# Performance work log

Measured on AMD Instinct MI355X. Metric: run time of the kernel, lower is better.

Reference implementation:

```python
import jax, jax.numpy as jnp
import numpy as np

B, D, R, E, L = 8192, 2048, 64, 4, 3


def setup_inputs() -> dict:
    key = jax.random.key(0)
    ks = jax.random.split(key, 6)
    inputs = jax.random.normal(ks[0], (B, D), dtype=jnp.float32)
    # xavier-normal-ish init for low-rank factors
    U = jax.random.normal(ks[1], (L, E, D, R), dtype=jnp.float32) * (2.0 / (D + R)) ** 0.5
    V = jax.random.normal(ks[2], (L, E, D, R), dtype=jnp.float32) * (2.0 / (D + R)) ** 0.5
    C = jax.random.normal(ks[3], (L, E, R, R), dtype=jnp.float32) * (1.0 / R) ** 0.5
    gate_w = jax.random.normal(ks[4], (E, D), dtype=jnp.float32) * (1.0 / D) ** 0.5
    bias = jnp.zeros((L, D), dtype=jnp.float32)
    return {"inputs": inputs, "U": U, "V": V, "C": C, "gate_w": gate_w, "bias": bias}


def reference(inputs, U, V, C, gate_w, bias):
    x0 = inputs                      # (B, D)
    x_l = inputs
    for i in range(L):
        # gating scores per expert, softmax over experts
        gs = jax.nn.softmax(x_l @ gate_w.T, axis=-1)            # (B, E)
        # low-rank cross: tanh(V^T x) -> tanh(C .) -> U .
        vx = jnp.tanh(jnp.einsum('edr,bd->ber', V[i], x_l))     # (B, E, R)
        cx = jnp.tanh(jnp.einsum('esr,ber->bes', C[i], vx))     # (B, E, R)
        uv = jnp.einsum('eds,bes->bed', U[i], cx)               # (B, E, D)
        dot = (uv + bias[i][None, None, :]) * x0[:, None, :]    # (B, E, D)
        x_l = jnp.einsum('bed,be->bd', dot, gs) + x_l           # MoE combine + residual
    return x_l
```

## Files before the change

### kernel.cpp

```cpp
#include <hip/hip_runtime.h>
#include <cmath>

#define Bb 8192
#define Dd 2048
#define Rr 64
#define Ee 4
#define Ll 3

typedef __bf16 bf16x8 __attribute__((ext_vector_type(8)));
typedef float f32x4 __attribute__((ext_vector_type(4)));
typedef unsigned short u16x8 __attribute__((ext_vector_type(8)));
typedef unsigned short u16x4 __attribute__((ext_vector_type(4)));

__device__ __forceinline__ unsigned short f2bf(float f){
  unsigned u = __builtin_bit_cast(unsigned, f);
  u += 0x7fffu + ((u >> 16) & 1u);
  return (unsigned short)(u >> 16);
}
__device__ __forceinline__ float bf2f(unsigned short h){
  return __builtin_bit_cast(float, ((unsigned)h) << 16);
}

__global__ __launch_bounds__(256) void cast_x_k(const float* __restrict__ x,
                                                unsigned short* __restrict__ xb0){
  const int n4 = Bb * Dd / 4;
  for (int i = blockIdx.x * blockDim.x + threadIdx.x; i < n4; i += gridDim.x * blockDim.x){
    f32x4 v = *((const f32x4*)x + i);
    u16x4 o;
    o[0] = f2bf(v[0]); o[1] = f2bf(v[1]); o[2] = f2bf(v[2]); o[3] = f2bf(v[3]);
    *((u16x4*)xb0 + i) = o;
  }
}

__global__ __launch_bounds__(256) void prep_w_k(const float* __restrict__ U,
                                                const float* __restrict__ V,
                                                const float* __restrict__ C,
                                                const float* __restrict__ gw,
                                                unsigned short* __restrict__ VfT,
                                                unsigned short* __restrict__ UfT,
                                                unsigned short* __restrict__ cb16,
                                                unsigned short* __restrict__ gw16){
  const int NV = Ll * 256 * Dd;
  const int NU = Ll * Dd * 256;
  const int NC = Ll * Ee * Rr * Rr;
  const int NG = Ee * Dd;
  const int total = NV + NU + NC + NG;
  for (int idx = blockIdx.x * blockDim.x + threadIdx.x; idx < total; idx += gridDim.x * blockDim.x){
    if (idx < NV){
      int l = idx / (256 * Dd); int rem = idx - l * 256 * Dd;
      int n = rem / Dd, d = rem - n * Dd;
      int e = n >> 6, r = n & 63;
      VfT[idx] = f2bf(V[(((size_t)l * Ee + e) * Dd + d) * Rr + r]);
    } else if (idx < NV + NU){
      int j = idx - NV;
      int l = j / (Dd * 256); int rem = j - l * Dd * 256;
      int d = rem / 256, k = rem - d * 256;
      int e = k >> 6, s = k & 63;
      UfT[j] = f2bf(U[(((size_t)l * Ee + e) * Dd + d) * Rr + s]);
    } else if (idx < NV + NU + NC){
      int j = idx - NV - NU;
      cb16[j] = f2bf(C[j]);
    } else {
      int j = idx - NV - NU - NC;
      gw16[j] = f2bf(gw[j]);
    }
  }
}

template<bool AF32>
__global__ __launch_bounds__(256) void gate_k(const void* __restrict__ xv,
                                              const unsigned short* __restrict__ gw16,
                                              float* __restrict__ gs){
  const int lane = threadIdx.x & 63;
  const int w = threadIdx.x >> 6;
  const int row = blockIdx.x * 4 + w;
  float s0 = 0.f, s1 = 0.f, s2 = 0.f, s3 = 0.f;
  #pragma unroll
  for (int c = 0; c < 4; c++){
    const int k = c * 512 + lane * 8;
    float xf[8];
    if constexpr (AF32){
      const float* xr = (const float*)xv + (size_t)row * Dd + k;
      f32x4 v0 = *(const f32x4*)xr;
      f32x4 v1 = *(const f32x4*)(xr + 4);
      #pragma unroll
      for (int u = 0; u < 4; u++){ xf[u] = v0[u]; xf[4 + u] = v1[u]; }
    } else {
      u16x8 xvv = *(const u16x8*)((const unsigned short*)xv + (size_t)row * Dd + k);
      #pragma unroll
      for (int u = 0; u < 8; u++) xf[u] = bf2f(xvv[u]);
    }
    u16x8 g0v = *(const u16x8*)(gw16 + 0 * Dd + k);
    u16x8 g1v = *(const u16x8*)(gw16 + 1 * Dd + k);
    u16x8 g2v = *(const u16x8*)(gw16 + 2 * Dd + k);
    u16x8 g3v = *(const u16x8*)(gw16 + 3 * Dd + k);
    #pragma unroll
    for (int u = 0; u < 8; u++){
      s0 += xf[u] * bf2f(g0v[u]);
      s1 += xf[u] * bf2f(g1v[u]);
      s2 += xf[u] * bf2f(g2v[u]);
      s3 += xf[u] * bf2f(g3v[u]);
    }
  }
  #pragma unroll
  for (int m = 1; m < 64; m <<= 1){
    s0 += __shfl_xor(s0, m, 64);
    s1 += __shfl_xor(s1, m, 64);
    s2 += __shfl_xor(s2, m, 64);
    s3 += __shfl_xor(s3, m, 64);
  }
  if (lane == 0){
    float mx = fmaxf(fmaxf(s0, s1), fmaxf(s2, s3));
    float e0 = __expf(s0 - mx), e1 = __expf(s1 - mx), e2 = __expf(s2 - mx), e3 = __expf(s3 - mx);
    float inv = 1.f / (e0 + e1 + e2 + e3);
    f32x4 g; g[0] = e0 * inv; g[1] = e1 * inv; g[2] = e2 * inv; g[3] = e3 * inv;
    *(f32x4*)(gs + (size_t)row * 4) = g;
  }
}

template<bool AF32>
__global__ __launch_bounds__(256) void gemm1_k(const void* __restrict__ Av,
                                               const unsigned short* __restrict__ BT,
                                               unsigned short* __restrict__ vxp){
  const int bm0 = blockIdx.x * 64;
  const int bn0 = blockIdx.y * 128;
  const int z   = blockIdx.z;
  const int kc0 = z * 512;
  const int tid = threadIdx.x;
  const int lane = tid & 63;
  const int wv = tid >> 6;
  const int wm = wv >> 1, wn = wv & 1;

  __shared__ __align__(16) char smraw[27648];
  unsigned short (*As)[72] = (unsigned short (*)[72])smraw;
  unsigned short (*Bs)[72] = (unsigned short (*)[72])(smraw + 9216);
  float (*epi)[132] = (float (*)[132])smraw;

  f32x4 acc[2][4] = {};
  const int arow = tid >> 2;
  const int aseg = tid & 3;

  const float* Af = (const float*)Av;
  const unsigned short* Ab = (const unsigned short*)Av;

  f32x4 a4[4]; u16x8 ar[2]; u16x8 br[4];
  if constexpr (AF32){
    #pragma unroll
    for (int j = 0; j < 4; j++)
      a4[j] = *(const f32x4*)(Af + (size_t)(bm0 + arow) * Dd + kc0 + aseg * 16 + j * 4);
  } else {
    ar[0] = *(const u16x8*)(Ab + (size_t)(bm0 + arow) * Dd + kc0 + aseg * 16);
    ar[1] = *(const u16x8*)(Ab + (size_t)(bm0 + arow) * Dd + kc0 + aseg * 16 + 8);
  }
  br[0] = *(const u16x8*)(BT + (size_t)(bn0 + arow) * Dd + kc0 + aseg * 16);
  br[1] = *(const u16x8*)(BT + (size_t)(bn0 + arow) * Dd + kc0 + aseg * 16 + 8);
  br[2] = *(const u16x8*)(BT + (size_t)(bn0 + arow + 64) * Dd + kc0 + aseg * 16);
  br[3] = *(const u16x8*)(BT + (size_t)(bn0 + arow + 64) * Dd + kc0 + aseg * 16 + 8);

  for (int k0 = kc0; k0 < kc0 + 512; k0 += 64){
    __syncthreads();
    if constexpr (AF32){
      u16x8 av0, av1;
      #pragma unroll
      for (int j = 0; j < 4; j++){
        av0[j] = f2bf(a4[0][j]); av0[4 + j] = f2bf(a4[1][j]);
        av1[j] = f2bf(a4[2][j]); av1[4 + j] = f2bf(a4[3][j]);
      }
      *(u16x8*)(&As[arow][aseg * 16])     = av0;
      *(u16x8*)(&As[arow][aseg * 16 + 8]) = av1;
    } else {
      *(u16x8*)(&As[arow][aseg * 16])     = ar[0];
      *(u16x8*)(&As[arow][aseg * 16 + 8]) = ar[1];
    }
    *(u16x8*)(&Bs[arow][aseg * 16])          = br[0];
    *(u16x8*)(&Bs[arow][aseg * 16 + 8])      = br[1];
    *(u16x8*)(&Bs[arow + 64][aseg * 16])     = br[2];
    *(u16x8*)(&Bs[arow + 64][aseg * 16 + 8]) = br[3];
    __syncthreads();

    int kn = k0 + 64;
    if (kn < kc0 + 512){
      if constexpr (AF32){
        #pragma unroll
        for (int j = 0; j < 4; j++)
          a4[j] = *(const f32x4*)(Af + (size_t)(bm0 + arow) * Dd + kn + aseg * 16 + j * 4);
      } else {
        ar[0] = *(const u16x8*)(Ab + (size_t)(bm0 + arow) * Dd + kn + aseg * 16);
        ar[1] = *(const u16x8*)(Ab + (size_t)(bm0 + arow) * Dd + kn + aseg * 16 + 8);
      }
      br[0] = *(const u16x8*)(BT + (size_t)(bn0 + arow) * Dd + kn + aseg * 16);
      br[1] = *(const u16x8*)(BT + (size_t)(bn0 + arow) * Dd + kn + aseg * 16 + 8);
      br[2] = *(const u16x8*)(BT + (size_t)(bn0 + arow + 64) * Dd + kn + aseg * 16);
      br[3] = *(const u16x8*)(BT + (size_t)(bn0 + arow + 64) * Dd + kn + aseg * 16 + 8);
    }

    #pragma unroll
    for (int ks = 0; ks < 2; ks++){
      bf16x8 af[2];
      #pragma unroll
      for (int mi = 0; mi < 2; mi++)
        af[mi] = *reinterpret_cast<const bf16x8*>(&As[wm * 32 + mi * 16 + (lane & 15)][ks * 32 + (lane >> 4) * 8]);
      #pragma unroll
      for (int nj = 0; nj < 4; nj++){
        bf16x8 bfr = *reinterpret_cast<const bf16x8*>(&Bs[wn * 64 + nj * 16 + (lane & 15)][ks * 32 + (lane >> 4) * 8]);
        #pragma unroll
        for (int mi = 0; mi < 2; mi++)
          acc[mi][nj] = __builtin_amdgcn_mfma_f32_16x16x32_bf16(af[mi], bfr, acc[mi][nj], 0, 0, 0);
      }
    }
  }

  unsigned short* outz = vxp + (size_t)z * Bb * 256;
  #pragma unroll
  for (int h = 0; h < 2; h++){
    __syncthreads();
    if (wm == h){
      #pragma unroll
      for (int mi = 0; mi < 2; mi++)
        #pragma unroll
        for (int nj = 0; nj < 4; nj++)
          #pragma unroll
          for (int q = 0; q < 4; q++)
            epi[mi * 16 + (lane >> 4) * 4 + q][wn * 64 + nj * 16 + (lane & 15)] = acc[mi][nj][q];
    }
    __syncthreads();
    #pragma unroll
    for (int c = 0; c < 4; c++){
      int idx = c * 256 + tid;
      int r = idx >> 5;
      int col = (idx & 31) * 4;
      f32x4 v = *(const f32x4*)&epi[r][col];
      u16x4 ov;
      #pragma unroll
      for (int j = 0; j < 4; j++) ov[j] = f2bf(v[j]);
      *(u16x4*)(outz + (size_t)(bm0 + h * 32 + r) * 256 + bn0 + col) = ov;
    }
  }
}

template<bool FROMPLOG>
__global__ __launch_bounds__(256) void gemm2_k(const unsigned short* __restrict__ vxp,
                                               const unsigned short* __restrict__ cb,
                                               const float* __restrict__ gsb,
                                               const float* __restrict__ plog,
                                               unsigned short* __restrict__ wb){
  const int bm0 = blockIdx.x * 64;
  const int e   = blockIdx.y;
  const int tid = threadIdx.x;
  const int lane = tid & 63;
  const int wv = tid >> 6;
  const int wm = wv >> 1, wn = wv & 1;

  __shared__ __align__(16) char smraw[19456];
  unsigned short (*As)[72] = (unsigned short (*)[72])smraw;
  unsigned short (*Bs)[72] = (unsigned short (*)[72])(smraw + 9216);
  float (*gs_l)[4] = (float (*)[4])(smraw + 18432);
  unsigned short (*epi)[72] = (unsigned short (*)[72])smraw;

  if constexpr (FROMPLOG){
    int r = tid >> 2, q = tid & 3;
    f32x4 s = {0.f, 0.f, 0.f, 0.f};
    #pragma unroll
    for (int ci = 0; ci < 4; ci++)
      s += *(const f32x4*)(plog + ((size_t)(q * 4 + ci) * Bb + bm0 + r) * 4);
    #pragma unroll
    for (int j = 0; j < 4; j++){
      s[j] += __shfl_xor(s[j], 1, 64);
      s[j] += __shfl_xor(s[j], 2, 64);
    }
    if (q == 0){
      float mx = fmaxf(fmaxf(s[0], s[1]), fmaxf(s[2], s[3]));
      float e0 = __expf(s[0] - mx), e1 = __expf(s[1] - mx), e2 = __expf(s[2] - mx), e3 = __expf(s[3] - mx);
      float inv = 1.f / (e0 + e1 + e2 + e3);
      f32x4 g; g[0] = e0 * inv; g[1] = e1 * inv; g[2] = e2 * inv; g[3] = e3 * inv;
      *(f32x4*)&gs_l[r][0] = g;
    }
  } else {
    if (tid < 64) *(f32x4*)&gs_l[tid][0] = *(const f32x4*)(gsb + (size_t)(bm0 + tid) * 4);
  }

  const int arow = tid >> 2;
  const int aseg = tid & 3;

  float tv[16];
  #pragma unroll
  for (int j = 0; j < 16; j++) tv[j] = 0.f;
  #pragma unroll
  for (int z = 0; z < 4; z++){
    const unsigned short* vz = vxp + ((size_t)z * Bb + bm0 + arow) * 256 + e * 64 + aseg * 16;
    u16x8 p0 = *(const u16x8*)vz;
    u16x8 p1 = *(const u16x8*)(vz + 8);
    #pragma unroll
    for (int j = 0; j < 8; j++){ tv[j] += bf2f(p0[j]); tv[8 + j] += bf2f(p1[j]); }
  }
  u16x8 av0, av1;
  #pragma unroll
  for (int j = 0; j < 4; j++){
    av0[j] = f2bf(tanhf(tv[j]));     av0[4 + j] = f2bf(tanhf(tv[4 + j]));
    av1[j] = f2bf(tanhf(tv[8 + j])); av1[4 + j] = f2bf(tanhf(tv[12 + j]));
  }
  *(u16x8*)(&As[arow][aseg * 16]) = av0;
  *(u16x8*)(&As[arow][aseg * 16 + 8]) = av1;
  *(u16x8*)(&Bs[arow][aseg * 16])     = *(const u16x8*)(cb + e * 4096 + arow * 64 + aseg * 16);
  *(u16x8*)(&Bs[arow][aseg * 16 + 8]) = *(const u16x8*)(cb + e * 4096 + arow * 64 + aseg * 16 + 8);
  __syncthreads();

  f32x4 acc[2][2] = {};
  #pragma unroll
  for (int kk = 0; kk < 2; kk++){
    bf16x8 af[2];
    #pragma unroll
    for (int mi = 0; mi < 2; mi++)
      af[mi] = *reinterpret_cast<const bf16x8*>(&As[wm * 32 + mi * 16 + (lane & 15)][kk * 32 + (lane >> 4) * 8]);
    #pragma unroll
    for (int nj = 0; nj < 2; nj++){
      bf16x8 bfr = *reinterpret_cast<const bf16x8*>(&Bs[wn * 32 + nj * 16 + (lane & 15)][kk * 32 + (lane >> 4) * 8]);
      #pragma unroll
      for (int mi = 0; mi < 2; mi++)
        acc[mi][nj] = __builtin_amdgcn_mfma_f32_16x16x32_bf16(af[mi], bfr, acc[mi][nj], 0, 0, 0);
    }
  }

  __syncthreads();
  #pragma unroll
  for (int mi = 0; mi < 2; mi++)
    #pragma unroll
    for (int nj = 0; nj < 2; nj++)
      #pragma unroll
      for (int q = 0; q < 4; q++){
        int row = wm * 32 + mi * 16 + (lane >> 4) * 4 + q;
        int col = wn * 32 + nj * 16 + (lane & 15);
        float g = gs_l[row][e];
        epi[row][col] = f2bf(g * tanhf(acc[mi][nj][q]));
      }
  __syncthreads();
  #pragma unroll
  for (int c = 0; c < 2; c++){
    int idx = c * 256 + tid;
    int row = idx >> 3;
    int col = (idx & 7) * 8;
    *(u16x8*)(wb + (size_t)(bm0 + row) * 256 + e * 64 + col) = *(const u16x8*)(&epi[row][col]);
  }
}

template<int MODE, bool X0BF>
__global__ __launch_bounds__(256, 4) void gemm3_k(const unsigned short* __restrict__ A,
                                                  const unsigned short* __restrict__ BT,
                                                  const float* __restrict__ x0f,
                                                  const unsigned short* __restrict__ x0b,
                                                  unsigned short* __restrict__ xst,
                                                  const float* __restrict__ biasrow,
                                                  float* __restrict__ out,
                                                  const unsigned short* __restrict__ gw16,
                                                  float* __restrict__ plog){
  const int bm0 = blockIdx.x * 128;
  const int bn0 = blockIdx.y * 128;
  const int tid = threadIdx.x;
  const int lane = tid & 63;
  const int wv = tid >> 6;
  const int wm = wv >> 1, wn = wv & 1;

  __shared__ __align__(16) char smraw[20480];
  unsigned short (*As)[40] = (unsigned short (*)[40])smraw;
  unsigned short (*Bs)[40] = (unsigned short (*)[40])(smraw + 10240);
  float (*epi)[132] = (float (*)[132])smraw;

  f32x4 acc[4][4] = {};
  const int arow = tid >> 2;
  const int aseg = tid & 3;

  u16x8 ar0 = *(const u16x8*)(A + (size_t)(bm0 + arow) * 256 + aseg * 8);
  u16x8 ar1 = *(const u16x8*)(A + (size_t)(bm0 + arow + 64) * 256 + aseg * 8);
  u16x8 br0 = *(const u16x8*)(BT + (size_t)(bn0 + arow) * 256 + aseg * 8);
  u16x8 br1 = *(const u16x8*)(BT + (size_t)(bn0 + arow + 64) * 256 + aseg * 8);

  for (int k0 = 0; k0 < 256; k0 += 32){
    __syncthreads();
    *(u16x8*)(&As[arow][aseg * 8])      = ar0;
    *(u16x8*)(&As[arow + 64][aseg * 8]) = ar1;
    *(u16x8*)(&Bs[arow][aseg * 8])      = br0;
    *(u16x8*)(&Bs[arow + 64][aseg * 8]) = br1;
    __syncthreads();
    if (k0 + 32 < 256){
      ar0 = *(const u16x8*)(A + (size_t)(bm0 + arow) * 256 + k0 + 32 + aseg * 8);
      ar1 = *(const u16x8*)(A + (size_t)(bm0 + arow + 64) * 256 + k0 + 32 + aseg * 8);
      br0 = *(const u16x8*)(BT + (size_t)(bn0 + arow) * 256 + k0 + 32 + aseg * 8);
      br1 = *(const u16x8*)(BT + (size_t)(bn0 + arow + 64) * 256 + k0 + 32 + aseg * 8);
    }
    bf16x8 af[4];
    #pragma unroll
    for (int mi = 0; mi < 4; mi++)
      af[mi] = *reinterpret_cast<const bf16x8*>(&As[wm * 64 + mi * 16 + (lane & 15)][(lane >> 4) * 8]);
    #pragma unroll
    for (int nj = 0; nj < 4; nj++){
      bf16x8 bfr = *reinterpret_cast<const bf16x8*>(&Bs[wn * 64 + nj * 16 + (lane & 15)][(lane >> 4) * 8]);
      #pragma unroll
      for (int mi = 0; mi < 4; mi++)
        acc[mi][nj] = __builtin_amdgcn_mfma_f32_16x16x32_bf16(af[mi], bfr, acc[mi][nj], 0, 0, 0);
    }
  }

  #pragma unroll
  for (int h = 0; h < 4; h++){
    __syncthreads();
    if (wm == (h >> 1)){
      const int mib = (h & 1) * 2;
      #pragma unroll
      for (int m2 = 0; m2 < 2; m2++)
        #pragma unroll
        for (int nj = 0; nj < 4; nj++)
          #pragma unroll
          for (int q = 0; q < 4; q++)
            epi[m2 * 16 + (lane >> 4) * 4 + q][wn * 64 + nj * 16 + (lane & 15)] = acc[mib + m2][nj][q];
    }
    __syncthreads();
    #pragma unroll
    for (int c = 0; c < 4; c++){
      int idx = c * 256 + tid;
      int r = idx >> 5;
      int col = (idx & 31) * 4;
      int row = bm0 + h * 32 + r;
      size_t o = (size_t)row * Dd + bn0 + col;
      f32x4 y = *(const f32x4*)&epi[r][col];
      f32x4 bv = *(const f32x4*)(biasrow + bn0 + col);
      f32x4 x0v;
      if constexpr (X0BF){
        u16x4 xv = *(const u16x4*)(x0b + o);
        #pragma unroll
        for (int j = 0; j < 4; j++) x0v[j] = bf2f(xv[j]);
      } else {
        x0v = *(const f32x4*)(x0f + o);
      }
      f32x4 xo;
      if constexpr (MODE == 0){
        xo = x0v;
      } else {
        u16x4 xv = *(const u16x4*)(xst + o);
        #pragma unroll
        for (int j = 0; j < 4; j++) xo[j] = bf2f(xv[j]);
      }
      f32x4 xn;
      #pragma unroll
      for (int j = 0; j < 4; j++) xn[j] = xo[j] + x0v[j] * (bv[j] + y[j]);
      if constexpr (MODE == 2){
        *(f32x4*)(out + o) = xn;
      } else {
        u16x4 xnb;
        #pragma unroll
        for (int j = 0; j < 4; j++) xnb[j] = f2bf(xn[j]);
        *(u16x4*)(xst + o) = xnb;
      }
      if constexpr (MODE != 2){
        float s[4];
        #pragma unroll
        for (int e = 0; e < 4; e++){
          u16x4 gv = *(const u16x4*)(gw16 + (size_t)e * Dd + bn0 + col);
          s[e] = xn[0] * bf2f(gv[0]) + xn[1] * bf2f(gv[1])
               + xn[2] * bf2f(gv[2]) + xn[3] * bf2f(gv[3]);
        }
        #pragma unroll
        for (int m = 1; m < 32; m <<= 1)
          #pragma unroll
          for (int e = 0; e < 4; e++) s[e] += __shfl_xor(s[e], m, 64);
        if ((tid & 31) == 0){
          f32x4 pv; pv[0] = s[0]; pv[1] = s[1]; pv[2] = s[2]; pv[3] = s[3];
          *(f32x4*)(plog + ((size_t)blockIdx.y * Bb + row) * 4) = pv;
        }
      }
    }
  }
}

extern "C" void kernel_launch(void* const* d_in, const int* in_sizes, int n_in,
                              void* d_out, int out_size, void* d_ws, size_t ws_size,
                              hipStream_t stream){
  (void)in_sizes; (void)n_in; (void)out_size;
  const float* inp  = (const float*)d_in[0];
  const float* U    = (const float*)d_in[1];
  const float* V    = (const float*)d_in[2];
  const float* C    = (const float*)d_in[3];
  const float* gw   = (const float*)d_in[4];
  const float* bias = (const float*)d_in[5];
  float* out = (float*)d_out;

  char* ws = (char*)d_ws;
  size_t o = 0;
  unsigned short* xb  = (unsigned short*)(ws + o); o += (size_t)Bb * Dd * 2;
  unsigned short* vxp = (unsigned short*)(ws + o); o += (size_t)4 * Bb * 256 * 2;
  unsigned short* wb  = (unsigned short*)(ws + o); o += (size_t)Bb * 256 * 2;
  float*          gsb = (float*)(ws + o);          o += (size_t)Bb * 4 * 4;
  float*          plog= (float*)(ws + o);          o += (size_t)16 * Bb * 4 * 4;
  unsigned short* vft = (unsigned short*)(ws + o); o += (size_t)Ll * 256 * Dd * 2;
  unsigned short* uft = (unsigned short*)(ws + o); o += (size_t)Ll * Dd * 256 * 2;
  unsigned short* cb16= (unsigned short*)(ws + o); o += (size_t)Ll * Ee * Rr * Rr * 2;
  unsigned short* g16 = (unsigned short*)(ws + o); o += (size_t)Ee * Dd * 2;
  if (ws_size < o) return;
  unsigned short* x0b = nullptr;
  if (ws_size >= o + (size_t)Bb * Dd * 2){
    x0b = (unsigned short*)(ws + o); o += (size_t)Bb * Dd * 2;
  }
  const bool hx = (x0b != nullptr);

  prep_w_k<<<1024, 256, 0, stream>>>(U, V, C, gw, vft, uft, cb16, g16);
  if (hx) cast_x_k<<<2048, 256, 0, stream>>>(inp, x0b);

  for (int l = 0; l < Ll; l++){
    const unsigned short* vftl = vft + (size_t)l * 256 * Dd;
    const unsigned short* uftl = uft + (size_t)l * Dd * 256;
    const unsigned short* cbl  = cb16 + (size_t)l * Ee * Rr * Rr;
    const float* biasl = bias + (size_t)l * Dd;

    if (l == 0){
      if (hx){
        gate_k<false><<<Bb / 4, 256, 0, stream>>>(x0b, g16, gsb);
        gemm1_k<false><<<dim3(Bb / 64, 2, 4), 256, 0, stream>>>(x0b, vftl, vxp);
      } else {
        gate_k<true><<<Bb / 4, 256, 0, stream>>>(inp, g16, gsb);
        gemm1_k<true><<<dim3(Bb / 64, 2, 4), 256, 0, stream>>>(inp, vftl, vxp);
      }
      gemm2_k<false><<<dim3(Bb / 64, Ee), 256, 0, stream>>>(vxp, cbl, gsb, plog, wb);
    } else {
      gemm1_k<false><<<dim3(Bb / 64, 2, 4), 256, 0, stream>>>(xb, vftl, vxp);
      gemm2_k<true><<<dim3(Bb / 64, Ee), 256, 0, stream>>>(vxp, cbl, gsb, plog, wb);
    }

    dim3 g3(Bb / 128, Dd / 128);
    if (l == 0){
      if (hx) gemm3_k<0, true ><<<g3, 256, 0, stream>>>(wb, uftl, inp, x0b, xb, biasl, out, g16, plog);
      else    gemm3_k<0, false><<<g3, 256, 0, stream>>>(wb, uftl, inp, x0b, xb, biasl, out, g16, plog);
    } else if (l == 1){
      if (hx) gemm3_k<1, true ><<<g3, 256, 0, stream>>>(wb, uftl, inp, x0b, xb, biasl, out, g16, plog);
      else    gemm3_k<1, false><<<g3, 256, 0, stream>>>(wb, uftl, inp, x0b, xb, biasl, out, g16, plog);
    } else {
      if (hx) gemm3_k<2, true ><<<g3, 256, 0, stream>>>(wb, uftl, inp, x0b, xb, biasl, out, g16, plog);
      else    gemm3_k<2, false><<<g3, 256, 0, stream>>>(wb, uftl, inp, x0b, xb, biasl, out, g16, plog);
    }
  }
}
```

Baseline: 213.5 us.

## Fuse input bf16 cast with layer-0 gating and prefetch epilogue operands

Merges the fp32-to-bf16 cast of the input with the layer-0 gate/softmax computation into one kernel. The input is read once instead of being written and then re-read as bf16 by a separate gate kernel, and one launch is removed. The gate now uses fp32 inputs rather than rounded bf16, which slightly changes numerics. Separately, the gemm3 epilogue prefetches x0 and the state tile for the next half-tile into double-buffered registers before the barrier, so global load latency overlaps the LDS staging, at the cost of more registers.

```diff
diff --git a/kernel.cpp b/kernel.cpp
--- a/kernel.cpp
+++ b/kernel.cpp
@@ -19,17 +19,6 @@
 }
 __device__ __forceinline__ float bf2f(unsigned short h){
   return __builtin_bit_cast(float, ((unsigned)h) << 16);
-}
-
-__global__ __launch_bounds__(256) void cast_x_k(const float* __restrict__ x,
-                                                unsigned short* __restrict__ xb0){
-  const int n4 = Bb * Dd / 4;
-  for (int i = blockIdx.x * blockDim.x + threadIdx.x; i < n4; i += gridDim.x * blockDim.x){
-    f32x4 v = *((const f32x4*)x + i);
-    u16x4 o;
-    o[0] = f2bf(v[0]); o[1] = f2bf(v[1]); o[2] = f2bf(v[2]); o[3] = f2bf(v[3]);
-    *((u16x4*)xb0 + i) = o;
-  }
 }
 
 __global__ __launch_bounds__(256) void prep_w_k(const float* __restrict__ U,
@@ -67,8 +56,57 @@
   }
 }
 
-template<bool AF32>
-__global__ __launch_bounds__(256) void gate_k(const void* __restrict__ xv,
+__global__ __launch_bounds__(256) void cast_gate_k(const float* __restrict__ x,
+                                                   unsigned short* __restrict__ xb0,
+                                                   const unsigned short* __restrict__ gw16,
+                                                   float* __restrict__ gs){
+  const int lane = threadIdx.x & 63;
+  const int w = threadIdx.x >> 6;
+  const int row = blockIdx.x * 4 + w;
+  float s0 = 0.f, s1 = 0.f, s2 = 0.f, s3 = 0.f;
+  #pragma unroll
+  for (int c = 0; c < 4; c++){
+    const int k = c * 512 + lane * 8;
+    const float* xr = x + (size_t)row * Dd + k;
+    f32x4 v0 = *(const f32x4*)xr;
+    f32x4 v1 = *(const f32x4*)(xr + 4);
+    float xf[8];
+    u16x8 ob;
+    #pragma unroll
+    for (int u = 0; u < 4; u++){
+      xf[u] = v0[u]; xf[4 + u] = v1[u];
+      ob[u] = f2bf(v0[u]); ob[4 + u] = f2bf(v1[u]);
+    }
+    *(u16x8*)(xb0 + (size_t)row * Dd + k) = ob;
+    u16x8 g0v = *(const u16x8*)(gw16 + 0 * Dd + k);
+    u16x8 g1v = *(const u16x8*)(gw16 + 1 * Dd + k);
+    u16x8 g2v = *(const u16x8*)(gw16 + 2 * Dd + k);
+    u16x8 g3v = *(const u16x8*)(gw16 + 3 * Dd + k);
+    #pragma unroll
+    for (int u = 0; u < 8; u++){
+      s0 += xf[u] * bf2f(g0v[u]);
+      s1 += xf[u] * bf2f(g1v[u]);
+      s2 += xf[u] * bf2f(g2v[u]);
+      s3 += xf[u] * bf2f(g3v[u]);
+    }
+  }
+  #pragma unroll
+  for (int m = 1; m < 64; m <<= 1){
+    s0 += __shfl_xor(s0, m, 64);
+    s1 += __shfl_xor(s1, m, 64);
+    s2 += __shfl_xor(s2, m, 64);
+    s3 += __shfl_xor(s3, m, 64);
+  }
+  if (lane == 0){
+    float mx = fmaxf(fmaxf(s0, s1), fmaxf(s2, s3));
+    float e0 = __expf(s0 - mx), e1 = __expf(s1 - mx), e2 = __expf(s2 - mx), e3 = __expf(s3 - mx);
+    float inv = 1.f / (e0 + e1 + e2 + e3);
+    f32x4 g; g[0] = e0 * inv; g[1] = e1 * inv; g[2] = e2 * inv; g[3] = e3 * inv;
+    *(f32x4*)(gs + (size_t)row * 4) = g;
+  }
+}
+
+__global__ __launch_bounds__(256) void gate_k(const float* __restrict__ xv,
                                               const unsigned short* __restrict__ gw16,
                                               float* __restrict__ gs){
   const int lane = threadIdx.x & 63;
@@ -78,18 +116,12 @@
   #pragma unroll
   for (int c = 0; c < 4; c++){
     const int k = c * 512 + lane * 8;
+    const float* xr = xv + (size_t)row * Dd + k;
+    f32x4 v0 = *(const f32x4*)xr;
+    f32x4 v1 = *(const f32x4*)(xr + 4);
     float xf[8];
-    if constexpr (AF32){
-      const float* xr = (const float*)xv + (size_t)row * Dd + k;
-      f32x4 v0 = *(const f32x4*)xr;
-      f32x4 v1 = *(const f32x4*)(xr + 4);
-      #pragma unroll
-      for (int u = 0; u < 4; u++){ xf[u] = v0[u]; xf[4 + u] = v1[u]; }
-    } else {
-      u16x8 xvv = *(const u16x8*)((const unsigned short*)xv + (size_t)row * Dd + k);
-      #pragma unroll
-      for (int u = 0; u < 8; u++) xf[u] = bf2f(xvv[u]);
-    }
+    #pragma unroll
+    for (int u = 0; u < 4; u++){ xf[u] = v0[u]; xf[4 + u] = v1[u]; }
     u16x8 g0v = *(const u16x8*)(gw16 + 0 * Dd + k);
     u16x8 g1v = *(const u16x8*)(gw16 + 1 * Dd + k);
     u16x8 g2v = *(const u16x8*)(gw16 + 2 * Dd + k);
@@ -400,6 +432,24 @@
     }
   }
 
+  u16x4 x0p[2][4]; u16x4 xsp[2][4]; f32x4 x0q[2][4];
+  (void)x0p; (void)xsp; (void)x0q;
+
+#define PRE_LOADS(H, S)                                                        \
+  {                                                                            \
+    _Pragma("unroll")                                                          \
+    for (int c = 0; c < 4; c++){                                               \
+      int idx = c * 256 + tid;                                                 \
+      int r = idx >> 5, col = (idx & 31) * 4;                                  \
+      size_t o = (size_t)(bm0 + (H) * 32 + r) * Dd + bn0 + col;                \
+      if constexpr (X0BF) x0p[S][c] = *(const u16x4*)(x0b + o);                \
+      else                x0q[S][c] = *(const f32x4*)(x0f + o);                \
+      if constexpr (MODE != 0) xsp[S][c] = *(const u16x4*)(xst + o);           \
+    }                                                                          \
+  }
+
+  PRE_LOADS(0, 0)
+
   #pragma unroll
   for (int h = 0; h < 4; h++){
     __syncthreads();
@@ -413,7 +463,11 @@
           for (int q = 0; q < 4; q++)
             epi[m2 * 16 + (lane >> 4) * 4 + q][wn * 64 + nj * 16 + (lane & 15)] = acc[mib + m2][nj][q];
     }
-    __syncthreads();
+    if (h == 0) PRE_LOADS(1, 1)
+    else if (h == 1) PRE_LOADS(2, 0)
+    else if (h == 2) PRE_LOADS(3, 1)
+    __syncthreads();
+    const int hb = h & 1;
     #pragma unroll
     for (int c = 0; c < 4; c++){
       int idx = c * 256 + tid;
@@ -425,17 +479,17 @@
       f32x4 bv = *(const f32x4*)(biasrow + bn0 + col);
       f32x4 x0v;
       if constexpr (X0BF){
-        u16x4 xv = *(const u16x4*)(x0b + o);
+        u16x4 xv = x0p[hb][c];
         #pragma unroll
         for (int j = 0; j < 4; j++) x0v[j] = bf2f(xv[j]);
       } else {
-        x0v = *(const f32x4*)(x0f + o);
+        x0v = x0q[hb][c];
       }
       f32x4 xo;
       if constexpr (MODE == 0){
         xo = x0v;
       } else {
-        u16x4 xv = *(const u16x4*)(xst + o);
+        u16x4 xv = xsp[hb][c];
         #pragma unroll
         for (int j = 0; j < 4; j++) xo[j] = bf2f(xv[j]);
       }
@@ -469,6 +523,7 @@
       }
     }
   }
+#undef PRE_LOADS
 }
 
 extern "C" void kernel_launch(void* const* d_in, const int* in_sizes, int n_in,
@@ -502,7 +557,7 @@
   const bool hx = (x0b != nullptr);
 
   prep_w_k<<<1024, 256, 0, stream>>>(U, V, C, gw, vft, uft, cb16, g16);
-  if (hx) cast_x_k<<<2048, 256, 0, stream>>>(inp, x0b);
+  if (hx) cast_gate_k<<<Bb / 4, 256, 0, stream>>>(inp, x0b, g16, gsb);
 
   for (int l = 0; l < Ll; l++){
     const unsigned short* vftl = vft + (size_t)l * 256 * Dd;
@@ -512,10 +567,9 @@
 
     if (l == 0){
       if (hx){
-        gate_k<false><<<Bb / 4, 256, 0, stream>>>(x0b, g16, gsb);
         gemm1_k<false><<<dim3(Bb / 64, 2, 4), 256, 0, stream>>>(x0b, vftl, vxp);
       } else {
-        gate_k<true><<<Bb / 4, 256, 0, stream>>>(inp, g16, gsb);
+        gate_k<<<Bb / 4, 256, 0, stream>>>(inp, g16, gsb);
         gemm1_k<true><<<dim3(Bb / 64, 2, 4), 256, 0, stream>>>(inp, vftl, vxp);
       }
       gemm2_k<false><<<dim3(Bb / 64, Ee), 256, 0, stream>>>(vxp, cbl, gsb, plog, wb);
```

Measured after the change: 239.6 us. 1.12x slower.
